# Optimization experiments

Hardware: AMD Instinct MI355X
Metric: run time of the kernel (lower is better)

The kernel has to match this reference:

```python
import jax, jax.numpy as jnp
import numpy as np

N = 100000      # nodes
E = 1600000     # edges (before self loops)
F_IN = 256      # num_features
HID = 8         # hid per head, layer 1
H1 = 8          # in_head
H2 = 4          # out_head
NCLS = 40       # num_classes


def setup_inputs() -> dict:
    key = jax.random.key(0)
    ks = jax.random.split(key, 10)
    p = lambda k, shape: jax.random.normal(k, shape, jnp.float32) * 0.1
    d1 = H1 * HID   # 64
    d2 = H2 * NCLS  # 160
    return dict(
        x=jax.random.normal(ks[0], (N, F_IN), jnp.float32),
        edge_index=jax.random.randint(ks[1], (2, E), 0, N),
        Wl1=p(ks[2], (F_IN, d1)), bl1=jnp.zeros((d1,), jnp.float32),
        Wr1=p(ks[3], (F_IN, d1)), br1=jnp.zeros((d1,), jnp.float32),
        att1=p(ks[4], (H1, HID)), b1=jnp.zeros((d1,), jnp.float32),
        Wl2=p(ks[5], (d1, d2)), bl2=jnp.zeros((d2,), jnp.float32),
        Wr2=p(ks[6], (d1, d2)), br2=jnp.zeros((d2,), jnp.float32),
        att2=p(ks[7], (H2, NCLS)), b2=jnp.zeros((NCLS,), jnp.float32),
    )


def gatv2_conv(x, src, dst, Wl, bl, Wr, br, att, bias, heads, ch, concat):
    """PyG GATv2Conv (eval mode): lin_l -> source/messages, lin_r -> target."""
    n = x.shape[0]
    xl = (x @ Wl + bl).reshape(n, heads, ch)   # source-side features
    xr = (x @ Wr + br).reshape(n, heads, ch)   # target-side features
    # edge-wise attention logits: LeakyReLU(x_i + x_j) . att
    e = jax.nn.leaky_relu(xl[src] + xr[dst], 0.2)          # [E, H, C]
    logits = jnp.einsum('ehc,hc->eh', e, att)               # [E, H]
    # segment softmax over incoming edges of each destination node
    m = jax.ops.segment_max(logits, dst, num_segments=n)    # [N, H]
    ex = jnp.exp(logits - m[dst])
    s = jax.ops.segment_sum(ex, dst, num_segments=n)        # [N, H]
    alpha = ex / (s[dst] + 1e-16)                           # [E, H]
    # scatter-add weighted source messages
    out = jax.ops.segment_sum(xl[src] * alpha[:, :, None], dst, num_segments=n)  # [N, H, C]
    if concat:
        return out.reshape(n, heads * ch) + bias
    return out.mean(axis=1) + bias


def reference(x, edge_index, Wl1, bl1, Wr1, br1, att1, b1,
              Wl2, bl2, Wr2, br2, att2, b2):
    n = x.shape[0]
    loop = jnp.arange(n)
    # PyG GATv2Conv default add_self_loops=True
    src = jnp.concatenate([edge_index[0], loop])
    dst = jnp.concatenate([edge_index[1], loop])
    # eval mode: all dropout (input, inter-layer, attention) disabled
    h = gatv2_conv(x, src, dst, Wl1, bl1, Wr1, br1, att1, b1, H1, HID, True)
    h = jax.nn.elu(h)
    out = gatv2_conv(h, src, dst, Wl2, bl2, Wr2, br2, att2, b2, H2, NCLS, False)
    return jax.nn.log_softmax(out, axis=1)
```

## Files before the change

kernel.cpp:

```cpp
#include <hip/hip_runtime.h>
#include <math.h>

#define NN 100000
#define EE 1600000
#define FIN 256
#define D1 64
#define D2 160
#define C2 40
#define P1R 72
#define P2R 192
#define PK1 264
#define PK2 72
#define NBUCK 391
#define CAP 5000
#define WSCL 0.015625f
#define L2E 1.442695041f
#define RB1 (P1R*2)
#define RB2 (P2R*2)

typedef unsigned short u16;
typedef __attribute__((ext_vector_type(8))) short bf16x8;
typedef __attribute__((ext_vector_type(4))) float f32x4;
typedef _Float16 h2t __attribute__((ext_vector_type(2)));
union hu { unsigned u; h2t h; };

__device__ __forceinline__ u16 f2bf(float f){
  unsigned b = __float_as_uint(f);
  return (u16)((b + 0x7FFFu + ((b >> 16) & 1u)) >> 16);
}
__device__ __forceinline__ u16 f2h(float f){
  union { _Float16 h; u16 u; } c; c.h = (_Float16)f; return c.u;
}
__device__ __forceinline__ float h16f(u16 v){
  union { u16 u; _Float16 h; } c; c.u = v; return (float)c.h;
}

__global__ void wprep_k(const float* __restrict__ Wl1, const float* __restrict__ Wr1,
                        const float* __restrict__ att1,
                        const float* __restrict__ bl1, const float* __restrict__ br1,
                        const float* __restrict__ Wl2, const float* __restrict__ Wr2,
                        const float* __restrict__ att2,
                        const float* __restrict__ bl2, const float* __restrict__ br2,
                        float* __restrict__ WA1, float* __restrict__ BA1,
                        float* __restrict__ WA2, float* __restrict__ BA2){
  int t = blockIdx.x*256 + threadIdx.x;
  if (t < 4096){
    int k = t >> 4, j = t & 15;
    float v = 0.f;
    if (j < 8){
      float s = 0.f;
      #pragma unroll
      for (int c = 0; c < 8; ++c) s += Wl1[(size_t)k*D1 + j*8 + c] * att1[j*8 + c];
      v = 0.6f * s;
    }
    WA1[t] = v;
  } else if (t < 4608){
    int i = t - 4096;
    int k = i >> 3, j = i & 7;
    float v = 0.f;
    if (j < 4){
      float s = 0.f;
      #pragma unroll
      for (int c = 0; c < 40; ++c) s += Wl2[(size_t)k*D2 + j*40 + c] * att2[j*40 + c];
      v = 0.6f * s;
    }
    WA2[i] = v;
  } else if (t < 4616){
    int j = t - 4608;
    float s = 0.f;
    #pragma unroll
    for (int c = 0; c < 8; ++c) s += bl1[j*8 + c] * att1[j*8 + c];
    BA1[j] = 0.6f * s;
  } else if (t < 4620){
    int j = t - 4616;
    float s = 0.f;
    #pragma unroll
    for (int c = 0; c < 40; ++c) s += bl2[j*40 + c] * att2[j*40 + c];
    BA2[j] = 0.6f * s;
  }
}

__global__ __launch_bounds__(256) void part1_k(const int* __restrict__ ei,
                                               int* __restrict__ bcnt,
                                               int* __restrict__ csrtmp){
  __shared__ int hist[NBUCK];
  __shared__ int gbase[NBUCK];
  int t = threadIdx.x;
  for (int i = t; i < NBUCK; i += 256) hist[i] = 0;
  __syncthreads();
  int rb[8], rr[8], rv[8];
  #pragma unroll
  for (int q = 0; q < 8; ++q){
    int e = blockIdx.x*2048 + q*256 + t;
    rb[q] = -1;
    if (e < EE){
      int s = ei[e], d = ei[EE + e];
      int b = d >> 8;
      rb[q] = b;
      rv[q] = s | ((d & 255) << 17);
      rr[q] = atomicAdd(&hist[b], 1);
    }
  }
  __syncthreads();
  for (int i = t; i < NBUCK; i += 256)
    if (hist[i] > 0) gbase[i] = atomicAdd(&bcnt[i], hist[i]);
  __syncthreads();
  #pragma unroll
  for (int q = 0; q < 8; ++q){
    if (rb[q] >= 0){
      int pos = gbase[rb[q]] + rr[q];
      if (pos < CAP) csrtmp[rb[q]*CAP + pos] = rv[q];
    }
  }
}

__global__ __launch_bounds__(256) void sort_k(const int* __restrict__ bcnt,
                                              const int* __restrict__ csrtmp,
                                              int* __restrict__ csr1,
                                              int* __restrict__ csr2,
                                              int* __restrict__ off,
                                              int* __restrict__ end){
  __shared__ int cnt[256];
  __shared__ int sc[256];
  __shared__ int cur[256];
  int b = blockIdx.x, t = threadIdx.x;
  int E = bcnt[b]; if (E > CAP) E = CAP;
  int n = (b << 8) + t;
  cnt[t] = (n < NN) ? 1 : 0;
  __syncthreads();
  for (int i = t; i < E; i += 256){
    int v = csrtmp[b*CAP + i];
    atomicAdd(&cnt[(v >> 17) & 255], 1);
  }
  __syncthreads();
  int x = cnt[t];
  sc[t] = x;
  __syncthreads();
  for (int o = 1; o < 256; o <<= 1){
    int v = (t >= o) ? sc[t - o] : 0;
    __syncthreads();
    sc[t] += v;
    __syncthreads();
  }
  int excl = sc[t] - x;
  if (n < NN){
    off[n] = b*CAP + excl;
    end[n] = b*CAP + excl + x;
    csr1[b*CAP + excl] = n * RB1;
    csr2[b*CAP + excl] = n * RB2;
    cur[t] = excl + 1;
  } else {
    cur[t] = excl;
  }
  __syncthreads();
  for (int i = t; i < E; i += 256){
    int v = csrtmp[b*CAP + i];
    int p = atomicAdd(&cur[(v >> 17) & 255], 1);
    int src = v & 0x1FFFF;
    csr1[b*CAP + p] = src * RB1;
    csr2[b*CAP + p] = src * RB2;
  }
}

__global__ __launch_bounds__(256) void gemm1_mfma(
    const float* __restrict__ X,
    const float* __restrict__ Wl, const float* __restrict__ bl,
    const float* __restrict__ Wr, const float* __restrict__ br,
    const float* __restrict__ WA1, const float* __restrict__ BA1,
    u16* __restrict__ outl, u16* __restrict__ outr){
  __shared__ u16 WB[144*PK1];
  int t = threadIdx.x;
  #pragma unroll
  for (int q = 0; q < 16; ++q){
    int idx = t + 256*q;
    int k = idx >> 4, c4 = idx & 15;
    float4 vl = *reinterpret_cast<const float4*>(Wl + (size_t)k*D1 + c4*4);
    float4 vr = *reinterpret_cast<const float4*>(Wr + (size_t)k*D1 + c4*4);
    WB[(c4*4+0)*PK1 + k] = f2bf(vl.x); WB[(c4*4+1)*PK1 + k] = f2bf(vl.y);
    WB[(c4*4+2)*PK1 + k] = f2bf(vl.z); WB[(c4*4+3)*PK1 + k] = f2bf(vl.w);
    WB[(64+c4*4+0)*PK1 + k] = f2bf(vr.x); WB[(64+c4*4+1)*PK1 + k] = f2bf(vr.y);
    WB[(64+c4*4+2)*PK1 + k] = f2bf(vr.z); WB[(64+c4*4+3)*PK1 + k] = f2bf(vr.w);
  }
  #pragma unroll
  for (int q = 0; q < 16; ++q){
    int idx = t + 256*q;
    int k = idx >> 4, j = idx & 15;
    WB[(128+j)*PK1 + k] = f2bf(WA1[k*16 + j]);
  }
  __syncthreads();
  int w = t >> 6, l = t & 63;
  int g = l >> 4;
  int arow = blockIdx.x*64 + w*16 + (l & 15);
  if (arow >= NN) arow = NN-1;
  const float* xp = X + (size_t)arow*FIN + g*8;
  f32x4 acc[9] = {};
  #pragma unroll
  for (int kk = 0; kk < 8; ++kk){
    float4 a0 = *reinterpret_cast<const float4*>(xp + kk*32);
    float4 a1 = *reinterpret_cast<const float4*>(xp + kk*32 + 4);
    union { bf16x8 v; u16 u[8]; } A;
    A.u[0]=f2bf(a0.x); A.u[1]=f2bf(a0.y); A.u[2]=f2bf(a0.z); A.u[3]=f2bf(a0.w);
    A.u[4]=f2bf(a1.x); A.u[5]=f2bf(a1.y); A.u[6]=f2bf(a1.z); A.u[7]=f2bf(a1.w);
    const u16* wb = WB + (l & 15)*PK1 + kk*32 + g*8;
    #pragma unroll
    for (int c = 0; c < 9; ++c){
      bf16x8 B = *reinterpret_cast<const bf16x8*>(wb + c*16*PK1);
      acc[c] = __builtin_amdgcn_mfma_f32_16x16x32_bf16(A.v, B, acc[c], 0, 0, 0);
    }
  }
  int ocol = l & 15;
  int orow0 = blockIdx.x*64 + w*16 + g*4;
  #pragma unroll
  for (int c = 0; c < 8; ++c){
    bool left = (c < 4);
    int col = (left ? c : c-4)*16 + ocol;
    u16* op = left ? outl : outr;
    float bv = (left ? bl : br)[col];
    #pragma unroll
    for (int r = 0; r < 4; ++r){
      int row = orow0 + r;
      if (row < NN) op[(size_t)row*P1R + col] = f2h(acc[c][r] + bv);
    }
  }
  if (ocol < 8){
    float bav = BA1[ocol];
    #pragma unroll
    for (int r = 0; r < 4; ++r){
      int row = orow0 + r;
      if (row < NN) outl[(size_t)row*P1R + 64 + ocol] = f2h(__expf(acc[8][r] + bav) * WSCL);
    }
  }
}

__global__ __launch_bounds__(256) void gemm2_mfma(
    const u16* __restrict__ H,
    const float* __restrict__ Wl, const float* __restrict__ bl,
    const float* __restrict__ Wr, const float* __restrict__ br,
    const float* __restrict__ WA2, const float* __restrict__ BA2,
    u16* __restrict__ outl, u16* __restrict__ outr){
  __shared__ u16 WB[336*PK2];
  int t = threadIdx.x;
  #pragma unroll
  for (int q = 0; q < 10; ++q){
    int idx = t + 256*q;
    int k = idx / 40, c4 = idx % 40;
    float4 vl = *reinterpret_cast<const float4*>(Wl + (size_t)k*D2 + c4*4);
    float4 vr = *reinterpret_cast<const float4*>(Wr + (size_t)k*D2 + c4*4);
    WB[(c4*4+0)*PK2 + k] = f2bf(vl.x); WB[(c4*4+1)*PK2 + k] = f2bf(vl.y);
    WB[(c4*4+2)*PK2 + k] = f2bf(vl.z); WB[(c4*4+3)*PK2 + k] = f2bf(vl.w);
    WB[(160+c4*4+0)*PK2 + k] = f2bf(vr.x); WB[(160+c4*4+1)*PK2 + k] = f2bf(vr.y);
    WB[(160+c4*4+2)*PK2 + k] = f2bf(vr.z); WB[(160+c4*4+3)*PK2 + k] = f2bf(vr.w);
  }
  #pragma unroll
  for (int q = 0; q < 2; ++q){
    int i2 = t + 256*q;
    int k = i2 >> 3, j = i2 & 7;
    WB[(320+j)*PK2 + k] = f2bf(WA2[k*8 + j]);
    WB[(328+j)*PK2 + k] = 0;
  }
  __syncthreads();
  int w = t >> 6, l = t & 63;
  int g = l >> 4;
  int arow = blockIdx.x*64 + w*16 + (l & 15);
  if (arow >= NN) arow = NN-1;
  const u16* hp = H + (size_t)arow*D1 + g*8;
  f32x4 acc[21] = {};
  #pragma unroll
  for (int kk = 0; kk < 2; ++kk){
    bf16x8 A = *reinterpret_cast<const bf16x8*>(hp + kk*32);
    const u16* wb = WB + (l & 15)*PK2 + kk*32 + g*8;
    #pragma unroll
    for (int c = 0; c < 21; ++c){
      bf16x8 B = *reinterpret_cast<const bf16x8*>(wb + c*16*PK2);
      acc[c] = __builtin_amdgcn_mfma_f32_16x16x32_bf16(A, B, acc[c], 0, 0, 0);
    }
  }
  int ocol = l & 15;
  int orow0 = blockIdx.x*64 + w*16 + g*4;
  #pragma unroll
  for (int c = 0; c < 20; ++c){
    bool left = (c < 10);
    int col = (left ? c : c-10)*16 + ocol;
    u16* op = left ? outl : outr;
    float bv = (left ? bl : br)[col];
    #pragma unroll
    for (int r = 0; r < 4; ++r){
      int row = orow0 + r;
      if (row < NN) op[(size_t)row*P2R + col] = f2h(acc[c][r] + bv);
    }
  }
  if (ocol < 4){
    float bav = BA2[ocol];
    #pragma unroll
    for (int r = 0; r < 4; ++r){
      int row = orow0 + r;
      if (row < NN) outl[(size_t)row*P2R + 160 + ocol] = f2h(__expf(acc[20][r] + bav) * WSCL);
    }
  }
}

__global__ void l1_fused(const u16* __restrict__ xl, const u16* __restrict__ xr,
                         const int* __restrict__ off, const int* __restrict__ end,
                         const int* __restrict__ csr1,
                         const float* __restrict__ att,
                         const float* __restrict__ b, u16* __restrict__ out){
  int tid = threadIdx.x;
  int lane = tid & 63;
  int g = (lane >> 4) & 1, l = lane & 15;
  int n = blockIdx.x*8 + (tid >> 6)*2 + (lane >> 5);
  if (n >= NN) return;
  int h = l >> 1;
  const char* xlb = (const char*)xl;
  int lo = 8*l;
  int wo = 128 + 2*h;
  uint2 xru = *reinterpret_cast<const uint2*>(xr + (size_t)n*P1R + 4*l);
  hu r0, r1; r0.u = xru.x; r1.u = xru.y;
  hu a0, a1;
  a0.h[0] = (_Float16)(0.4f*L2E*att[4*l+0]); a0.h[1] = (_Float16)(0.4f*L2E*att[4*l+1]);
  a1.h[0] = (_Float16)(0.4f*L2E*att[4*l+2]); a1.h[1] = (_Float16)(0.4f*L2E*att[4*l+3]);
  float s = 0.f;
  hu acc0, acc1; acc0.u = 0; acc1.u = 0;
  int p = off[n] + g, e1 = end[n];
  for (; p + 6 < e1; p += 8){
    unsigned bo[4];
    #pragma unroll
    for (int q = 0; q < 4; ++q) bo[q] = (unsigned)csr1[p + 2*q];
    uint2 uv[4]; u16 wv[4];
    #pragma unroll
    for (int q = 0; q < 4; ++q){
      uv[q] = *reinterpret_cast<const uint2*>(xlb + bo[q] + lo);
      wv[q] = *reinterpret_cast<const u16*>(xlb + bo[q] + wo);
    }
    #pragma unroll
    for (int q = 0; q < 4; ++q){
      hu x0, x1; x0.u = uv[q].x; x1.u = uv[q].y;
      hu y0, y1; y0.h = x0.h + r0.h; y1.h = x1.h + r1.h;
      y0.u &= 0x7FFF7FFFu; y1.u &= 0x7FFF7FFFu;
      hu t2; t2.h = a0.h*y0.h + a1.h*y1.h;
      float tf = (float)t2.h[0] + (float)t2.h[1];
      tf += __shfl_xor(tf, 1);
      float pa = __builtin_amdgcn_exp2f(tf) * h16f(wv[q]);
      s += pa;
      hu pp; pp.h[0] = (_Float16)pa; pp.h[1] = pp.h[0];
      acc0.h = pp.h*x0.h + acc0.h;
      acc1.h = pp.h*x1.h + acc1.h;
    }
  }
  for (; p < e1; p += 2){
    unsigned bo = (unsigned)csr1[p];
    uint2 ua = *reinterpret_cast<const uint2*>(xlb + bo + lo);
    u16 wa = *reinterpret_cast<const u16*>(xlb + bo + wo);
    hu x0, x1; x0.u = ua.x; x1.u = ua.y;
    hu y0, y1; y0.h = x0.h + r0.h; y1.h = x1.h + r1.h;
    y0.u &= 0x7FFF7FFFu; y1.u &= 0x7FFF7FFFu;
    hu t2; t2.h = a0.h*y0.h + a1.h*y1.h;
    float tf = (float)t2.h[0] + (float)t2.h[1];
    tf += __shfl_xor(tf, 1);
    float pa = __builtin_amdgcn_exp2f(tf) * h16f(wa);
    s += pa;
    hu pp; pp.h[0] = (_Float16)pa; pp.h[1] = pp.h[0];
    acc0.h = pp.h*x0.h + acc0.h;
    acc1.h = pp.h*x1.h + acc1.h;
  }
  s += __shfl_xor(s, 16);
  { hu m; m.u = (unsigned)__shfl_xor((int)acc0.u, 16); acc0.h = acc0.h + m.h; }
  { hu m; m.u = (unsigned)__shfl_xor((int)acc1.u, 16); acc1.h = acc1.h + m.h; }
  if (g == 0){
    float inv = 1.f / (s + 1e-16f);
    float v0 = (float)acc0.h[0]*inv + b[4*l+0];
    float v1 = (float)acc0.h[1]*inv + b[4*l+1];
    float v2 = (float)acc1.h[0]*inv + b[4*l+2];
    float v3 = (float)acc1.h[1]*inv + b[4*l+3];
    ushort4 o;
    o.x = f2bf(v0 > 0.f ? v0 : expm1f(v0));
    o.y = f2bf(v1 > 0.f ? v1 : expm1f(v1));
    o.z = f2bf(v2 > 0.f ? v2 : expm1f(v2));
    o.w = f2bf(v3 > 0.f ? v3 : expm1f(v3));
    *reinterpret_cast<ushort4*>(out + (size_t)n*D1 + 4*l) = o;
  }
}

__global__ void l2_fused(const u16* __restrict__ xl, const u16* __restrict__ xr,
                         const int* __restrict__ off, const int* __restrict__ end,
                         const int* __restrict__ csr2,
                         const float* __restrict__ att,
                         const float* __restrict__ b, float* __restrict__ out){
  int tid = threadIdx.x;
  int lane = tid & 63;
  int g = (lane >> 4) & 1, l = lane & 15;
  int n = blockIdx.x*8 + (tid >> 6)*2 + (lane >> 5);
  if (n >= NN) return;
  int h = l >> 2;
  int c0 = 10*l;
  const char* xlb = (const char*)xl;
  int lo = 20*l;
  int wo = 320 + 2*h;
  hu xr2[5], a2[5];
  #pragma unroll
  for (int d = 0; d < 5; ++d){
    xr2[d].u = *reinterpret_cast<const unsigned*>(xr + (size_t)n*P2R + c0 + 2*d);
    a2[d].h[0] = (_Float16)(0.4f*L2E*att[c0 + 2*d]);
    a2[d].h[1] = (_Float16)(0.4f*L2E*att[c0 + 2*d + 1]);
  }
  float s = 0.f;
  hu acc2[5];
  #pragma unroll
  for (int d = 0; d < 5; ++d) acc2[d].u = 0;
  int p = off[n] + g, e1 = end[n];
  for (; p + 6 < e1; p += 8){
    unsigned bo[4];
    #pragma unroll
    for (int q = 0; q < 4; ++q) bo[q] = (unsigned)csr2[p + 2*q];
    hu xa[4][5]; u16 wv[4];
    #pragma unroll
    for (int q = 0; q < 4; ++q){
      const char* rp = xlb + bo[q] + lo;
      #pragma unroll
      for (int d = 0; d < 5; ++d) xa[q][d].u = *reinterpret_cast<const unsigned*>(rp + 4*d);
      wv[q] = *reinterpret_cast<const u16*>(xlb + bo[q] + wo);
    }
    #pragma unroll
    for (int q = 0; q < 4; ++q){
      hu t2; t2.u = 0;
      #pragma unroll
      for (int d = 0; d < 5; ++d){
        hu y; y.h = xa[q][d].h + xr2[d].h; y.u &= 0x7FFF7FFFu;
        t2.h = a2[d].h*y.h + t2.h;
      }
      float tf = (float)t2.h[0] + (float)t2.h[1];
      tf += __shfl_xor(tf, 1); tf += __shfl_xor(tf, 2);
      float pa = __builtin_amdgcn_exp2f(tf) * h16f(wv[q]);
      s += pa;
      hu pp; pp.h[0] = (_Float16)pa; pp.h[1] = pp.h[0];
      #pragma unroll
      for (int d = 0; d < 5; ++d) acc2[d].h = pp.h*xa[q][d].h + acc2[d].h;
    }
  }
  for (; p < e1; p += 2){
    unsigned bo = (unsigned)csr2[p];
    const char* rp = xlb + bo + lo;
    hu xa[5];
    #pragma unroll
    for (int d = 0; d < 5; ++d) xa[d].u = *reinterpret_cast<const unsigned*>(rp + 4*d);
    u16 wa16 = *reinterpret_cast<const u16*>(xlb + bo + wo);
    hu ta2; ta2.u = 0;
    #pragma unroll
    for (int d = 0; d < 5; ++d){
      hu ya; ya.h = xa[d].h + xr2[d].h; ya.u &= 0x7FFF7FFFu;
      ta2.h = a2[d].h*ya.h + ta2.h;
    }
    float ta = (float)ta2.h[0] + (float)ta2.h[1];
    ta += __shfl_xor(ta, 1); ta += __shfl_xor(ta, 2);
    float pa = __builtin_amdgcn_exp2f(ta) * h16f(wa16);
    s += pa;
    hu ppa; ppa.h[0] = (_Float16)pa; ppa.h[1] = ppa.h[0];
    #pragma unroll
    for (int d = 0; d < 5; ++d) acc2[d].h = ppa.h*xa[d].h + acc2[d].h;
  }
  s += __shfl_xor(s, 16);
  #pragma unroll
  for (int d = 0; d < 5; ++d){
    hu m; m.u = (unsigned)__shfl_xor((int)acc2[d].u, 16);
    acc2[d].h = acc2[d].h + m.h;
  }
  float inv = 1.f / (s + 1e-16f);
  float v[10];
  #pragma unroll
  for (int d = 0; d < 5; ++d){
    v[2*d]   = (float)acc2[d].h[0] * inv;
    v[2*d+1] = (float)acc2[d].h[1] * inv;
  }
  #pragma unroll
  for (int k = 0; k < 10; ++k){
    float o = v[k];
    o += __shfl_xor(o, 4);
    o += __shfl_xor(o, 8);
    v[k] = o*0.25f + b[10*(l & 3) + k];
  }
  float mx = v[0];
  #pragma unroll
  for (int k = 1; k < 10; ++k) mx = fmaxf(mx, v[k]);
  mx = fmaxf(mx, __shfl_xor(mx, 1));
  mx = fmaxf(mx, __shfl_xor(mx, 2));
  float es = 0.f;
  #pragma unroll
  for (int k = 0; k < 10; ++k) es += __expf(v[k] - mx);
  es += __shfl_xor(es, 1);
  es += __shfl_xor(es, 2);
  float lse = mx + __logf(es);
  if (g == 0 && l < 4){
    float* op = out + (size_t)n*C2 + 10*l;
    #pragma unroll
    for (int k2 = 0; k2 < 5; ++k2)
      *reinterpret_cast<float2*>(op + 2*k2) = make_float2(v[2*k2] - lse, v[2*k2+1] - lse);
  }
}

extern "C" void kernel_launch(void* const* d_in, const int* in_sizes, int n_in,
                              void* d_out, int out_size, void* d_ws, size_t ws_size,
                              hipStream_t stream){
  const float* x    = (const float*)d_in[0];
  const int*   ei   = (const int*)  d_in[1];
  const float* Wl1  = (const float*)d_in[2];
  const float* bl1  = (const float*)d_in[3];
  const float* Wr1  = (const float*)d_in[4];
  const float* br1  = (const float*)d_in[5];
  const float* att1 = (const float*)d_in[6];
  const float* b1   = (const float*)d_in[7];
  const float* Wl2  = (const float*)d_in[8];
  const float* bl2  = (const float*)d_in[9];
  const float* Wr2  = (const float*)d_in[10];
  const float* br2  = (const float*)d_in[11];
  const float* att2 = (const float*)d_in[12];
  const float* b2   = (const float*)d_in[13];
  float* out = (float*)d_out;

  char* ws = (char*)d_ws;
  u16*   B1     = (u16*)  (ws);
  u16*   B2     = (u16*)  (ws + 15000000);
  u16*   h1     = (u16*)  (ws + 30000000);
  u16*   B3     = (u16*)  (ws + 43000000);
  u16*   B4     = (u16*)  (ws + 82000000);
  int*   csrtmp = (int*)  (ws + 82000000);
  float* WA1    = (float*)(ws + 121000000);
  float* BA1    = (float*)(ws + 121100000);
  float* WA2    = (float*)(ws + 121200000);
  float* BA2    = (float*)(ws + 121300000);
  int*   off    = (int*)  (ws + 121400000);
  int*   end    = (int*)  (ws + 121900000);
  int*   bcnt   = (int*)  (ws + 122400000);
  int*   csr1   = (int*)  (ws + 122500000);
  int*   csr2   = (int*)  (ws + 130400000);
  const int blk = 256;
  const int MB = (NN + 63)/64;

  hipMemsetAsync(bcnt, 0, (size_t)NBUCK*4, stream);
  part1_k<<<(EE + 2047)/2048, blk, 0, stream>>>(ei, bcnt, csrtmp);
  sort_k <<<NBUCK, blk, 0, stream>>>(bcnt, csrtmp, csr1, csr2, off, end);
  wprep_k<<<19, blk, 0, stream>>>(Wl1, Wr1, att1, bl1, br1,
                                  Wl2, Wr2, att2, bl2, br2, WA1, BA1, WA2, BA2);

  gemm1_mfma<<<MB, blk, 0, stream>>>(x, Wl1, bl1, Wr1, br1, WA1, BA1, B1, B2);
  l1_fused  <<<(NN + 7)/8, blk, 0, stream>>>(B1, B2, off, end, csr1, att1, b1, h1);

  gemm2_mfma<<<MB, blk, 0, stream>>>(h1, Wl2, bl2, Wr2, br2, WA2, BA2, B3, B4);
  l2_fused  <<<(NN + 7)/8, blk, 0, stream>>>(B3, B4, off, end, csr2, att2, b2, out);
}
```

Baseline: 365.2 us.

## Pre-partition edges by source block before destination bucketing for gather locality

Adds a first pass that partitions edges into coarse source-node superbuckets, then runs the destination bucketing from those partitions. Within each destination bucket, edges are then roughly ordered by source, so the later gathers of source rows should hit cache better. It also shrinks the P2R row pitch from 192 to 168, which reduces the layer-2 feature buffer footprint. The cost is an extra full pass over the edges and a larger temporary buffer, and any superbucket that overflows its capacity silently drops edges.

```diff
diff --git a/kernel.cpp b/kernel.cpp
--- a/kernel.cpp
+++ b/kernel.cpp
@@ -8,11 +8,14 @@
 #define D2 160
 #define C2 40
 #define P1R 72
-#define P2R 192
+#define P2R 168
 #define PK1 264
 #define PK2 72
 #define NBUCK 391
 #define CAP 5000
+#define NSB 25
+#define CAPS 68000
+#define BPB 34
 #define WSCL 0.015625f
 #define L2E 1.442695041f
 #define RB1 (P1R*2)
@@ -80,24 +83,60 @@
   }
 }
 
-__global__ __launch_bounds__(256) void part1_k(const int* __restrict__ ei,
+__global__ __launch_bounds__(256) void psortA_k(const int* __restrict__ ei,
+                                                int* __restrict__ pcnt,
+                                                int2* __restrict__ ptmp){
+  __shared__ int hist[NSB];
+  __shared__ int gbase[NSB];
+  int t = threadIdx.x;
+  if (t < NSB) hist[t] = 0;
+  __syncthreads();
+  int rb[8], rr[8]; int2 rv[8];
+  #pragma unroll
+  for (int q = 0; q < 8; ++q){
+    int e = blockIdx.x*2048 + q*256 + t;
+    rb[q] = -1;
+    if (e < EE){
+      int s = ei[e], d = ei[EE + e];
+      int b = s >> 12;
+      rb[q] = b;
+      rv[q] = make_int2(s, d);
+      rr[q] = atomicAdd(&hist[b], 1);
+    }
+  }
+  __syncthreads();
+  if (t < NSB && hist[t] > 0) gbase[t] = atomicAdd(&pcnt[t], hist[t]);
+  __syncthreads();
+  #pragma unroll
+  for (int q = 0; q < 8; ++q){
+    if (rb[q] >= 0){
+      int pos = gbase[rb[q]] + rr[q];
+      if (pos < CAPS) ptmp[(size_t)rb[q]*CAPS + pos] = rv[q];
+    }
+  }
+}
+
+__global__ __launch_bounds__(256) void part1_k(const int2* __restrict__ ptmp,
+                                               const int* __restrict__ pcnt,
                                                int* __restrict__ bcnt,
                                                int* __restrict__ csrtmp){
   __shared__ int hist[NBUCK];
   __shared__ int gbase[NBUCK];
   int t = threadIdx.x;
+  int sb = blockIdx.x / BPB, sl = blockIdx.x % BPB;
+  int cnt = pcnt[sb]; if (cnt > CAPS) cnt = CAPS;
   for (int i = t; i < NBUCK; i += 256) hist[i] = 0;
   __syncthreads();
   int rb[8], rr[8], rv[8];
   #pragma unroll
   for (int q = 0; q < 8; ++q){
-    int e = blockIdx.x*2048 + q*256 + t;
+    int i = sl*2048 + q*256 + t;
     rb[q] = -1;
-    if (e < EE){
-      int s = ei[e], d = ei[EE + e];
-      int b = d >> 8;
+    if (i < cnt){
+      int2 sd = ptmp[(size_t)sb*CAPS + i];
+      int b = sd.y >> 8;
       rb[q] = b;
-      rv[q] = s | ((d & 255) << 17);
+      rv[q] = sd.x | ((sd.y & 255) << 17);
       rr[q] = atomicAdd(&hist[b], 1);
     }
   }
@@ -520,25 +559,29 @@
   u16*   B2     = (u16*)  (ws + 15000000);
   u16*   h1     = (u16*)  (ws + 30000000);
   u16*   B3     = (u16*)  (ws + 43000000);
-  u16*   B4     = (u16*)  (ws + 82000000);
-  int*   csrtmp = (int*)  (ws + 82000000);
-  float* WA1    = (float*)(ws + 121000000);
-  float* BA1    = (float*)(ws + 121100000);
-  float* WA2    = (float*)(ws + 121200000);
-  float* BA2    = (float*)(ws + 121300000);
-  int*   off    = (int*)  (ws + 121400000);
-  int*   end    = (int*)  (ws + 121900000);
-  int*   bcnt   = (int*)  (ws + 122400000);
-  int*   csr1   = (int*)  (ws + 122500000);
-  int*   csr2   = (int*)  (ws + 130400000);
+  u16*   B4     = (u16*)  (ws + 77000000);
+  int*   csrtmp = (int*)  (ws + 77000000);
+  int2*  ptmp   = (int2*) (ws + 86000000);
+  float* WA1    = (float*)(ws + 111000000);
+  float* BA1    = (float*)(ws + 111100000);
+  float* WA2    = (float*)(ws + 111200000);
+  float* BA2    = (float*)(ws + 111300000);
+  int*   off    = (int*)  (ws + 111400000);
+  int*   end    = (int*)  (ws + 111900000);
+  int*   bcnt   = (int*)  (ws + 112400000);
+  int*   pcnt   = (int*)  (ws + 112450000);
+  int*   csr1   = (int*)  (ws + 112500000);
+  int*   csr2   = (int*)  (ws + 120400000);
   const int blk = 256;
   const int MB = (NN + 63)/64;
 
   hipMemsetAsync(bcnt, 0, (size_t)NBUCK*4, stream);
-  part1_k<<<(EE + 2047)/2048, blk, 0, stream>>>(ei, bcnt, csrtmp);
-  sort_k <<<NBUCK, blk, 0, stream>>>(bcnt, csrtmp, csr1, csr2, off, end);
-  wprep_k<<<19, blk, 0, stream>>>(Wl1, Wr1, att1, bl1, br1,
-                                  Wl2, Wr2, att2, bl2, br2, WA1, BA1, WA2, BA2);
+  hipMemsetAsync(pcnt, 0, (size_t)NSB*4, stream);
+  psortA_k<<<(EE + 2047)/2048, blk, 0, stream>>>(ei, pcnt, ptmp);
+  part1_k <<<NSB*BPB, blk, 0, stream>>>(ptmp, pcnt, bcnt, csrtmp);
+  sort_k  <<<NBUCK, blk, 0, stream>>>(bcnt, csrtmp, csr1, csr2, off, end);
+  wprep_k <<<19, blk, 0, stream>>>(Wl1, Wr1, att1, bl1, br1,
+                                   Wl2, Wr2, att2, bl2, br2, WA1, BA1, WA2, BA2);
 
   gemm1_mfma<<<MB, blk, 0, stream>>>(x, Wl1, bl1, Wr1, br1, WA1, BA1, B1, B2);
   l1_fused  <<<(NN + 7)/8, blk, 0, stream>>>(B1, B2, off, end, csr1, att1, b1, h1);
```

Result: no change. 371.1 us (+1.6%).
